# Kernel tuning notes

Hardware: AMD Instinct MI355X
Metric: run time of the kernel (lower is better)

Reference implementation:

```python
import jax, jax.numpy as jnp
import numpy as np

N = 100000
E = 300000
IN_C = 256
HID = 256   # 2 * out_channels
OUT_C = 128


def setup_inputs() -> dict:
    key = jax.random.key(0)
    k1, k2, k3, k4, k5 = jax.random.split(key, 5)
    x = jax.random.normal(k1, (N, IN_C), dtype=jnp.float32)
    edge_index = jax.random.randint(k2, (2, E), 0, N, dtype=jnp.int64)
    # Glorot-style init scale for GEMM weights
    W1 = jax.random.normal(k3, (IN_C, HID), dtype=jnp.float32) * (1.0 / np.sqrt(IN_C))
    b1 = jnp.zeros((HID,), dtype=jnp.float32)
    W2 = jax.random.normal(k4, (HID, OUT_C), dtype=jnp.float32) * (1.0 / np.sqrt(HID))
    b2 = jnp.zeros((OUT_C,), dtype=jnp.float32)
    return {"x": x, "edge_index": edge_index, "W1": W1, "b1": b1, "W2": W2, "b2": b2}


def _gcn_conv(x, W, b, src, dst, norm, n_nodes):
    # x: [N, Fin] -> transform then gather-scale-scatter aggregate
    h = x @ W                                   # [N, Fout]
    msgs = h[src] * norm[:, None]               # [E+N, Fout] (includes self-loops)
    out = jax.ops.segment_sum(msgs, dst, num_segments=n_nodes)
    return out + b


def _gcn_norm(edge_index, n_nodes):
    # add self-loops, compute symmetric deg^-1/2 normalization (PyG GCNConv default)
    loops = jnp.arange(n_nodes, dtype=edge_index.dtype)
    src = jnp.concatenate([edge_index[0], loops])
    dst = jnp.concatenate([edge_index[1], loops])
    deg = jax.ops.segment_sum(jnp.ones_like(dst, dtype=jnp.float32), dst, num_segments=n_nodes)
    dinv = jnp.where(deg > 0, jax.lax.rsqrt(deg), 0.0)
    norm = dinv[src] * dinv[dst]                # [E+N]
    return src, dst, norm


def reference(x, edge_index, W1, b1, W2, b2):
    n_nodes = x.shape[0]
    src, dst, norm = _gcn_norm(edge_index, n_nodes)
    h = _gcn_conv(x, W1, b1, src, dst, norm, n_nodes)
    h = jax.nn.relu(h)
    # dropout is identity in eval mode (reference baseline runs deterministic eval)
    return _gcn_conv(h, W2, b2, src, dst, norm, n_nodes)
```

## Files before the change

### kernel.cpp

```cpp
#include <hip/hip_runtime.h>
#include <stdint.h>

#define IN_C  256
#define HID   256
#define OUT_C 128
#define SCAN_BS 1024

typedef __bf16 bf16x8 __attribute__((ext_vector_type(8)));
typedef float  f32x4  __attribute__((ext_vector_type(4)));
typedef unsigned short u16x8 __attribute__((ext_vector_type(8)));
typedef unsigned short u16x4 __attribute__((ext_vector_type(4)));
typedef unsigned short u16x2 __attribute__((ext_vector_type(2)));
typedef unsigned int u32;

static __device__ __forceinline__ unsigned short f2b(float f) {
    union { float f; uint32_t u; } v; v.f = f;
    uint32_t r = v.u + 0x7fffu + ((v.u >> 16) & 1u);
    return (unsigned short)(r >> 16);
}
static __device__ __forceinline__ float b2f(unsigned short b) {
    union { uint32_t u; float f; } v; v.u = ((uint32_t)b) << 16;
    return v.f;
}
static __device__ __forceinline__ u32 cvtpk(float lo, float hi) {
    u32 r;
    asm("v_cvt_pk_bf16_f32 %0, %1, %2" : "=v"(r) : "v"(lo), "v"(hi));
    return r;
}

typedef __attribute__((address_space(1))) const u32 gas_u32;
typedef __attribute__((address_space(3))) u32 las_u32;
static __device__ __forceinline__ void gld16(const void* g, void* l) {
    __builtin_amdgcn_global_load_lds((gas_u32*)g, (las_u32*)l, 16, 0, 0);
}

__global__ void k_init(const float* __restrict__ W1, const float* __restrict__ W2,
                       unsigned short* __restrict__ W1T, unsigned short* __restrict__ W2T,
                       int* __restrict__ cnt, int n) {
    int i = blockIdx.x * blockDim.x + threadIdx.x;
    if (i < 65536) W1T[i] = f2b(W1[(i & 255) * HID + (i >> 8)]);
    if (i < 32768) W2T[i] = f2b(W2[(i & 255) * OUT_C + (i >> 8)]);
    if (i < n) cnt[i] = 0;
}

__global__ void k_count(const int* __restrict__ dst, int* __restrict__ cnt, int e) {
    int i = blockIdx.x * blockDim.x + threadIdx.x;
    if (i < e) atomicAdd(&cnt[dst[i]], 1);
}

__global__ __launch_bounds__(SCAN_BS) void k_scan_block(
    const int* __restrict__ cnt, int* __restrict__ rs, int* __restrict__ bsum, int n) {
    __shared__ int s[SCAN_BS];
    const int tid = threadIdx.x;
    const int i = blockIdx.x * SCAN_BS + tid;
    int v = (i < n) ? cnt[i] + 1 : 0;
    s[tid] = v;
    __syncthreads();
    for (int off = 1; off < SCAN_BS; off <<= 1) {
        int t = (tid >= off) ? s[tid - off] : 0;
        __syncthreads();
        s[tid] += t;
        __syncthreads();
    }
    if (i < n) rs[i] = s[tid] - v;
    if (tid == SCAN_BS - 1) bsum[blockIdx.x] = s[tid];
}

__global__ void k_scan_sums(int* __restrict__ bsum, int nb) {
    __shared__ int s[128];
    const int tid = threadIdx.x;
    int v = (tid < nb) ? bsum[tid] : 0;
    s[tid] = v;
    __syncthreads();
    for (int off = 1; off < 128; off <<= 1) {
        int t = (tid >= off) ? s[tid - off] : 0;
        __syncthreads();
        s[tid] += t;
        __syncthreads();
    }
    if (tid < nb) bsum[tid] = s[tid] - v;
}

__global__ void k_scan_add(int* __restrict__ rs, int* __restrict__ cur,
                           const int* __restrict__ bsum, const int* __restrict__ cnt,
                           float* __restrict__ dinv, int2* __restrict__ csrw, int n) {
    int i = blockIdx.x * blockDim.x + threadIdx.x;
    if (i < n) {
        int v = rs[i] + bsum[i >> 10];
        rs[i] = v;
        cur[i] = v + 1;
        float dp1 = (float)(cnt[i] + 1);
        dinv[i] = rsqrtf(dp1);
        csrw[v] = make_int2(i, __float_as_int(1.0f / dp1));
    }
}

__global__ void k_fill(const int* __restrict__ src, const int* __restrict__ dst,
                       const float* __restrict__ dinv,
                       int* __restrict__ cur, int2* __restrict__ csrw, int e) {
    int i = blockIdx.x * blockDim.x + threadIdx.x;
    if (i < e) {
        int s = src[i], d = dst[i];
        int p = atomicAdd(&cur[d], 1);
        csrw[p] = make_int2(s, __float_as_int(dinv[s] * dinv[d]));
    }
}

__global__ __launch_bounds__(256) void k_gemm1(
    const float* __restrict__ x, const unsigned short* __restrict__ W1T,
    unsigned short* __restrict__ t1, int n) {
    __shared__ __align__(16) unsigned short As[128 * 64];
    __shared__ __align__(16) unsigned short Bs[128 * 64];
    const int tid  = threadIdx.x;
    const int bm = blockIdx.x >> 1, bn = blockIdx.x & 1;
    const int row0 = bm * 128, col0 = bn * 128;
    const int wid = tid >> 6, lane = tid & 63;
    const int wm = wid >> 1, wn = wid & 1;
    const int lrow = lane & 15, lgrp = lane >> 4;

    f32x4 acc[4][4];
    #pragma unroll
    for (int i = 0; i < 4; ++i)
        #pragma unroll
        for (int j = 0; j < 4; ++j)
            acc[i][j] = (f32x4){0.f, 0.f, 0.f, 0.f};

    for (int kt = 0; kt < 4; ++kt) {
        #pragma unroll
        for (int i = 0; i < 4; ++i) {
            int chunk = tid + 256 * i;
            int nn = chunk >> 3, c = chunk & 7;
            gld16(&W1T[(size_t)(col0 + nn) * 256 + kt * 64 + ((c ^ (nn & 7)) * 8)],
                  &Bs[chunk * 8]);
        }
        #pragma unroll
        for (int i = 0; i < 4; ++i) {
            int chunk = tid + 256 * i;
            int r = chunk >> 3, c = chunk & 7;
            int grow = row0 + r;
            union { u32 w[4]; u16x8 v; } pk;
            pk.w[0] = 0; pk.w[1] = 0; pk.w[2] = 0; pk.w[3] = 0;
            if (grow < n) {
                const float* sp = x + (size_t)grow * IN_C + kt * 64 + c * 8;
                f32x4 a = *(const f32x4*)sp;
                f32x4 b = *(const f32x4*)(sp + 4);
                pk.w[0] = cvtpk(a[0], a[1]); pk.w[1] = cvtpk(a[2], a[3]);
                pk.w[2] = cvtpk(b[0], b[1]); pk.w[3] = cvtpk(b[2], b[3]);
            }
            *(u16x8*)&As[r * 64 + ((c ^ (r & 7)) * 8)] = pk.v;
        }
        __syncthreads();
        #pragma unroll
        for (int kk = 0; kk < 2; ++kk) {
            const int cfrag = kk * 4 + lgrp;
            bf16x8 av[4], bv[4];
            #pragma unroll
            for (int mf = 0; mf < 4; ++mf) {
                int r = wm * 64 + mf * 16 + lrow;
                av[mf] = *(const bf16x8*)&As[r * 64 + ((cfrag ^ (r & 7)) * 8)];
            }
            #pragma unroll
            for (int nf = 0; nf < 4; ++nf) {
                int cc = wn * 64 + nf * 16 + lrow;
                bv[nf] = *(const bf16x8*)&Bs[cc * 64 + ((cfrag ^ (cc & 7)) * 8)];
            }
            #pragma unroll
            for (int mf = 0; mf < 4; ++mf)
                #pragma unroll
                for (int nf = 0; nf < 4; ++nf)
                    acc[mf][nf] = __builtin_amdgcn_mfma_f32_16x16x32_bf16(
                        av[mf], bv[nf], acc[mf][nf], 0, 0, 0);
        }
        __syncthreads();
    }
    #pragma unroll
    for (int mf = 0; mf < 4; ++mf)
        #pragma unroll
        for (int j = 0; j < 4; ++j) {
            int grow = row0 + wm * 64 + mf * 16 + lgrp * 4 + j;
            if (grow < n) {
                #pragma unroll
                for (int nf = 0; nf < 4; ++nf) {
                    int col = col0 + wn * 64 + nf * 16 + lrow;
                    t1[(size_t)grow * HID + col] = f2b(acc[mf][nf][j]);
                }
            }
        }
}

__global__ __launch_bounds__(256) void k_agg1(
    const unsigned short* __restrict__ t1, const int* __restrict__ rs,
    const int* __restrict__ cnt, const int2* __restrict__ csrw,
    const float* __restrict__ b1, unsigned short* __restrict__ out1, int n) {
    const int w = blockIdx.x * 4 + (threadIdx.x >> 6);
    const int n0 = w * 4;
    if (n0 >= n) return;
    const int lane = threadIdx.x & 63;
    const int ch = lane * 4;
    int beg[4], m[4];
    #pragma unroll
    for (int q = 0; q < 4; ++q) {
        int node = n0 + q;
        bool valid = node < n;
        beg[q] = valid ? rs[node] : 0;
        m[q]   = valid ? cnt[node] + 1 : 0;
    }
    float acc[4][4];
    #pragma unroll
    for (int q = 0; q < 4; ++q)
        #pragma unroll
        for (int k = 0; k < 4; ++k) acc[q][k] = 0.f;
    const int m01 = m[0] > m[1] ? m[0] : m[1];
    const int m23 = m[2] > m[3] ? m[2] : m[3];
    const int mmax = m01 > m23 ? m01 : m23;
    for (int j = 0; j < mmax; ++j) {
        #pragma unroll
        for (int q = 0; q < 4; ++q) {
            if (j < m[q]) {
                int2 p = csrw[beg[q] + j];
                float wq = __int_as_float(p.y);
                u16x4 u = *(const u16x4*)&t1[(size_t)p.x * HID + ch];
                acc[q][0] += b2f(u[0]) * wq; acc[q][1] += b2f(u[1]) * wq;
                acc[q][2] += b2f(u[2]) * wq; acc[q][3] += b2f(u[3]) * wq;
            }
        }
    }
    float4 bb = *(const float4*)(b1 + ch);
    #pragma unroll
    for (int q = 0; q < 4; ++q) {
        int node = n0 + q;
        if (node < n) {
            u16x4 o;
            o[0] = f2b(fmaxf(acc[q][0] + bb.x, 0.f));
            o[1] = f2b(fmaxf(acc[q][1] + bb.y, 0.f));
            o[2] = f2b(fmaxf(acc[q][2] + bb.z, 0.f));
            o[3] = f2b(fmaxf(acc[q][3] + bb.w, 0.f));
            *(u16x4*)&out1[(size_t)node * HID + ch] = o;
        }
    }
}

__global__ __launch_bounds__(256) void k_gemm2(
    const unsigned short* __restrict__ out1, const unsigned short* __restrict__ W2T,
    unsigned short* __restrict__ t2, int n) {
    __shared__ __align__(16) unsigned short As[128 * 64];
    __shared__ __align__(16) unsigned short Bs[128 * 64];
    const int tid  = threadIdx.x;
    const int row0 = blockIdx.x * 128;
    const int wid = tid >> 6, lane = tid & 63;
    const int wm = wid >> 1, wn = wid & 1;
    const int lrow = lane & 15, lgrp = lane >> 4;

    f32x4 acc[4][4];
    #pragma unroll
    for (int i = 0; i < 4; ++i)
        #pragma unroll
        for (int j = 0; j < 4; ++j)
            acc[i][j] = (f32x4){0.f, 0.f, 0.f, 0.f};

    for (int kt = 0; kt < 4; ++kt) {
        #pragma unroll
        for (int i = 0; i < 4; ++i) {
            int chunk = tid + 256 * i;
            int r = chunk >> 3, c = chunk & 7;
            int grow = row0 + r; if (grow > n - 1) grow = n - 1;
            gld16(&out1[(size_t)grow * HID + kt * 64 + ((c ^ (r & 7)) * 8)],
                  &As[chunk * 8]);
        }
        #pragma unroll
        for (int i = 0; i < 4; ++i) {
            int chunk = tid + 256 * i;
            int nn = chunk >> 3, c = chunk & 7;
            gld16(&W2T[(size_t)nn * 256 + kt * 64 + ((c ^ (nn & 7)) * 8)],
                  &Bs[chunk * 8]);
        }
        __syncthreads();
        #pragma unroll
        for (int kk = 0; kk < 2; ++kk) {
            const int cfrag = kk * 4 + lgrp;
            bf16x8 av[4], bv[4];
            #pragma unroll
            for (int mf = 0; mf < 4; ++mf) {
                int r = wm * 64 + mf * 16 + lrow;
                av[mf] = *(const bf16x8*)&As[r * 64 + ((cfrag ^ (r & 7)) * 8)];
            }
            #pragma unroll
            for (int nf = 0; nf < 4; ++nf) {
                int cc = wn * 64 + nf * 16 + lrow;
                bv[nf] = *(const bf16x8*)&Bs[cc * 64 + ((cfrag ^ (cc & 7)) * 8)];
            }
            #pragma unroll
            for (int mf = 0; mf < 4; ++mf)
                #pragma unroll
                for (int nf = 0; nf < 4; ++nf)
                    acc[mf][nf] = __builtin_amdgcn_mfma_f32_16x16x32_bf16(
                        av[mf], bv[nf], acc[mf][nf], 0, 0, 0);
        }
        __syncthreads();
    }
    #pragma unroll
    for (int mf = 0; mf < 4; ++mf)
        #pragma unroll
        for (int j = 0; j < 4; ++j) {
            int grow = row0 + wm * 64 + mf * 16 + lgrp * 4 + j;
            if (grow < n) {
                #pragma unroll
                for (int nf = 0; nf < 4; ++nf) {
                    int col = wn * 64 + nf * 16 + lrow;
                    t2[(size_t)grow * OUT_C + col] = f2b(acc[mf][nf][j]);
                }
            }
        }
}

__global__ __launch_bounds__(256) void k_agg2(
    const unsigned short* __restrict__ t2, const int* __restrict__ rs,
    const int* __restrict__ cnt, const int2* __restrict__ csrw,
    const float* __restrict__ b2, float* __restrict__ out, int n) {
    const int w = blockIdx.x * 4 + (threadIdx.x >> 6);
    const int n0 = w * 4;
    if (n0 >= n) return;
    const int lane = threadIdx.x & 63;
    const int ch = lane * 2;
    int beg[4], m[4];
    #pragma unroll
    for (int q = 0; q < 4; ++q) {
        int node = n0 + q;
        bool valid = node < n;
        beg[q] = valid ? rs[node] : 0;
        m[q]   = valid ? cnt[node] + 1 : 0;
    }
    float acc[4][2];
    #pragma unroll
    for (int q = 0; q < 4; ++q) { acc[q][0] = 0.f; acc[q][1] = 0.f; }
    const int m01 = m[0] > m[1] ? m[0] : m[1];
    const int m23 = m[2] > m[3] ? m[2] : m[3];
    const int mmax = m01 > m23 ? m01 : m23;
    for (int j = 0; j < mmax; ++j) {
        #pragma unroll
        for (int q = 0; q < 4; ++q) {
            if (j < m[q]) {
                int2 p = csrw[beg[q] + j];
                float wq = __int_as_float(p.y);
                u16x2 u = *(const u16x2*)&t2[(size_t)p.x * OUT_C + ch];
                acc[q][0] += b2f(u[0]) * wq; acc[q][1] += b2f(u[1]) * wq;
            }
        }
    }
    float2 bb = *(const float2*)(b2 + ch);
    #pragma unroll
    for (int q = 0; q < 4; ++q) {
        int node = n0 + q;
        if (node < n)
            *(float2*)&out[(size_t)node * OUT_C + ch] =
                make_float2(acc[q][0] + bb.x, acc[q][1] + bb.y);
    }
}

extern "C" void kernel_launch(void* const* d_in, const int* in_sizes, int n_in,
                              void* d_out, int out_size, void* d_ws, size_t ws_size,
                              hipStream_t stream) {
    const float* x  = (const float*)d_in[0];
    const int*   ei = (const int*)d_in[1];
    const float* W1 = (const float*)d_in[2];
    const float* b1 = (const float*)d_in[3];
    const float* W2 = (const float*)d_in[4];
    const float* b2 = (const float*)d_in[5];
    float* out = (float*)d_out;

    const int n = in_sizes[0] / IN_C;
    const int e = in_sizes[1] / 2;
    const int* src = ei;
    const int* dst = ei + e;

    int*   cnt  = (int*)d_ws;
    int*   rs   = cnt + n;
    int*   cur  = rs + n;
    int*   bsum = cur + n;
    float* dinv = (float*)(bsum + 128);
    int2*  csrw = (int2*)(dinv + n);
    unsigned short* W1T = (unsigned short*)(csrw + (size_t)e + n);
    unsigned short* W2T = W1T + 65536;
    unsigned short* t1  = W2T + 32768;
    unsigned short* out1 = t1 + (size_t)n * HID;
    unsigned short* t2  = t1;

    const int nb = (n + SCAN_BS - 1) / SCAN_BS;

    k_init<<<(n + 255) / 256, 256, 0, stream>>>(W1, W2, W1T, W2T, cnt, n);
    k_count<<<(e + 255) / 256, 256, 0, stream>>>(dst, cnt, e);
    k_scan_block<<<nb, SCAN_BS, 0, stream>>>(cnt, rs, bsum, n);
    k_scan_sums<<<1, 128, 0, stream>>>(bsum, nb);
    k_scan_add<<<(n + 255) / 256, 256, 0, stream>>>(rs, cur, bsum, cnt, dinv, csrw, n);
    k_fill<<<(e + 255) / 256, 256, 0, stream>>>(src, dst, dinv, cur, csrw, e);

    const int mb = (n + 127) / 128;
    k_gemm1<<<mb * 2, 256, 0, stream>>>(x, W1T, t1, n);
    const int aggblk = (n + 15) / 16;
    k_agg1<<<aggblk, 256, 0, stream>>>(t1, rs, cnt, csrw, b1, out1, n);
    k_gemm2<<<mb, 256, 0, stream>>>(out1, W2T, t2, n);
    k_agg2<<<aggblk, 256, 0, stream>>>(t2, rs, cnt, csrw, b2, out, n);
}
```

Before: 218.1 us.

## Restructure GEMM1 into full-width 512-thread tiles with double-buffered LDS prefetch

GEMM1 now has each block compute all 256 output columns for 128 rows with 8 waves, so x is read once instead of twice (the old grid split N in two). The K loop uses 32-wide steps with double-buffered LDS, prefetching the next W1 tile via global_load_lds and the next x slice into registers while MFMAs run on the current buffer. W1 is pre-packed in a k-chunked layout that matches the LDS layout, and the XOR swizzle is replaced by a column-chunk-major layout. Out-of-range rows are clamped instead of zero-filled. The trade-offs are more LDS per block, more sync points and possible bank conflicts in the new layout.

```diff
diff --git a/kernel.cpp b/kernel.cpp
--- a/kernel.cpp
+++ b/kernel.cpp
@@ -35,10 +35,15 @@
 }
 
 __global__ void k_init(const float* __restrict__ W1, const float* __restrict__ W2,
-                       unsigned short* __restrict__ W1T, unsigned short* __restrict__ W2T,
+                       unsigned short* __restrict__ W1G, unsigned short* __restrict__ W2T,
                        int* __restrict__ cnt, int n) {
     int i = blockIdx.x * blockDim.x + threadIdx.x;
-    if (i < 65536) W1T[i] = f2b(W1[(i & 255) * HID + (i >> 8)]);
+    if (i < 65536) {
+        int gi = i >> 3, j = i & 7;
+        int kt = gi >> 10, c = (gi >> 8) & 3, nn = gi & 255;
+        int k = kt * 32 + c * 8 + j;
+        W1G[i] = f2b(W1[(size_t)k * HID + nn]);
+    }
     if (i < 32768) W2T[i] = f2b(W2[(i & 255) * OUT_C + (i >> 8)]);
     if (i < n) cnt[i] = 0;
 }
@@ -106,17 +111,20 @@
     }
 }
 
-__global__ __launch_bounds__(256) void k_gemm1(
-    const float* __restrict__ x, const unsigned short* __restrict__ W1T,
+__global__ __launch_bounds__(512) void k_gemm1(
+    const float* __restrict__ x, const unsigned short* __restrict__ W1G,
     unsigned short* __restrict__ t1, int n) {
-    __shared__ __align__(16) unsigned short As[128 * 64];
-    __shared__ __align__(16) unsigned short Bs[128 * 64];
+    __shared__ __align__(16) unsigned short As[2][4096];
+    __shared__ __align__(16) unsigned short Bs[2][8192];
     const int tid  = threadIdx.x;
-    const int bm = blockIdx.x >> 1, bn = blockIdx.x & 1;
-    const int row0 = bm * 128, col0 = bn * 128;
+    const int row0 = blockIdx.x * 128;
     const int wid = tid >> 6, lane = tid & 63;
-    const int wm = wid >> 1, wn = wid & 1;
+    const int wm = wid >> 2, wn = wid & 3;
     const int lrow = lane & 15, lgrp = lane >> 4;
+
+    const int ar = tid & 127, ac = tid >> 7;
+    int arow = row0 + ar; if (arow > n - 1) arow = n - 1;
+    const float* aptr = x + (size_t)arow * IN_C + ac * 8;
 
     f32x4 acc[4][4];
     #pragma unroll
@@ -125,54 +133,63 @@
         for (int j = 0; j < 4; ++j)
             acc[i][j] = (f32x4){0.f, 0.f, 0.f, 0.f};
 
-    for (int kt = 0; kt < 4; ++kt) {
-        #pragma unroll
-        for (int i = 0; i < 4; ++i) {
-            int chunk = tid + 256 * i;
-            int nn = chunk >> 3, c = chunk & 7;
-            gld16(&W1T[(size_t)(col0 + nn) * 256 + kt * 64 + ((c ^ (nn & 7)) * 8)],
-                  &Bs[chunk * 8]);
-        }
-        #pragma unroll
-        for (int i = 0; i < 4; ++i) {
-            int chunk = tid + 256 * i;
-            int r = chunk >> 3, c = chunk & 7;
-            int grow = row0 + r;
+    {
+        #pragma unroll
+        for (int i = 0; i < 2; ++i) {
+            int chunk = tid + 512 * i;
+            gld16(&W1G[(size_t)chunk * 8], &Bs[0][chunk * 8]);
+        }
+        f32x4 a = *(const f32x4*)aptr;
+        f32x4 b = *(const f32x4*)(aptr + 4);
+        union { u32 w[4]; u16x8 v; } pk;
+        pk.w[0] = cvtpk(a[0], a[1]); pk.w[1] = cvtpk(a[2], a[3]);
+        pk.w[2] = cvtpk(b[0], b[1]); pk.w[3] = cvtpk(b[2], b[3]);
+        *(u16x8*)&As[0][ac * 1024 + ar * 8] = pk.v;
+    }
+    __syncthreads();
+
+    int cur = 0;
+    for (int kt = 0; kt < 8; ++kt) {
+        const int nxt = cur ^ 1;
+        f32x4 pa, pb;
+        const bool more = (kt < 7);
+        if (more) {
+            #pragma unroll
+            for (int i = 0; i < 2; ++i) {
+                int chunk = tid + 512 * i;
+                gld16(&W1G[(size_t)(kt + 1) * 8192 + chunk * 8], &Bs[nxt][chunk * 8]);
+            }
+            const float* ap = aptr + (kt + 1) * 32;
+            pa = *(const f32x4*)ap;
+            pb = *(const f32x4*)(ap + 4);
+        }
+        bf16x8 av[4], bv[4];
+        #pragma unroll
+        for (int mf = 0; mf < 4; ++mf) {
+            int r = wm * 64 + mf * 16 + lrow;
+            av[mf] = *(const bf16x8*)&As[cur][lgrp * 1024 + r * 8];
+        }
+        #pragma unroll
+        for (int nf = 0; nf < 4; ++nf) {
+            int cc = wn * 64 + nf * 16 + lrow;
+            bv[nf] = *(const bf16x8*)&Bs[cur][lgrp * 2048 + cc * 8];
+        }
+        #pragma unroll
+        for (int mf = 0; mf < 4; ++mf)
+            #pragma unroll
+            for (int nf = 0; nf < 4; ++nf)
+                acc[mf][nf] = __builtin_amdgcn_mfma_f32_16x16x32_bf16(
+                    av[mf], bv[nf], acc[mf][nf], 0, 0, 0);
+        if (more) {
             union { u32 w[4]; u16x8 v; } pk;
-            pk.w[0] = 0; pk.w[1] = 0; pk.w[2] = 0; pk.w[3] = 0;
-            if (grow < n) {
-                const float* sp = x + (size_t)grow * IN_C + kt * 64 + c * 8;
-                f32x4 a = *(const f32x4*)sp;
-                f32x4 b = *(const f32x4*)(sp + 4);
-                pk.w[0] = cvtpk(a[0], a[1]); pk.w[1] = cvtpk(a[2], a[3]);
-                pk.w[2] = cvtpk(b[0], b[1]); pk.w[3] = cvtpk(b[2], b[3]);
-            }
-            *(u16x8*)&As[r * 64 + ((c ^ (r & 7)) * 8)] = pk.v;
-        }
-        __syncthreads();
-        #pragma unroll
-        for (int kk = 0; kk < 2; ++kk) {
-            const int cfrag = kk * 4 + lgrp;
-            bf16x8 av[4], bv[4];
-            #pragma unroll
-            for (int mf = 0; mf < 4; ++mf) {
-                int r = wm * 64 + mf * 16 + lrow;
-                av[mf] = *(const bf16x8*)&As[r * 64 + ((cfrag ^ (r & 7)) * 8)];
-            }
-            #pragma unroll
-            for (int nf = 0; nf < 4; ++nf) {
-                int cc = wn * 64 + nf * 16 + lrow;
-                bv[nf] = *(const bf16x8*)&Bs[cc * 64 + ((cfrag ^ (cc & 7)) * 8)];
-            }
-            #pragma unroll
-            for (int mf = 0; mf < 4; ++mf)
-                #pragma unroll
-                for (int nf = 0; nf < 4; ++nf)
-                    acc[mf][nf] = __builtin_amdgcn_mfma_f32_16x16x32_bf16(
-                        av[mf], bv[nf], acc[mf][nf], 0, 0, 0);
-        }
-        __syncthreads();
-    }
+            pk.w[0] = cvtpk(pa[0], pa[1]); pk.w[1] = cvtpk(pa[2], pa[3]);
+            pk.w[2] = cvtpk(pb[0], pb[1]); pk.w[3] = cvtpk(pb[2], pb[3]);
+            *(u16x8*)&As[nxt][ac * 1024 + ar * 8] = pk.v;
+        }
+        __syncthreads();
+        cur = nxt;
+    }
+
     #pragma unroll
     for (int mf = 0; mf < 4; ++mf)
         #pragma unroll
@@ -181,7 +198,7 @@
             if (grow < n) {
                 #pragma unroll
                 for (int nf = 0; nf < 4; ++nf) {
-                    int col = col0 + wn * 64 + nf * 16 + lrow;
+                    int col = wn * 64 + nf * 16 + lrow;
                     t1[(size_t)grow * HID + col] = f2b(acc[mf][nf][j]);
                 }
             }
@@ -379,15 +396,15 @@
     int*   bsum = cur + n;
     float* dinv = (float*)(bsum + 128);
     int2*  csrw = (int2*)(dinv + n);
-    unsigned short* W1T = (unsigned short*)(csrw + (size_t)e + n);
-    unsigned short* W2T = W1T + 65536;
+    unsigned short* W1G = (unsigned short*)(csrw + (size_t)e + n);
+    unsigned short* W2T = W1G + 65536;
     unsigned short* t1  = W2T + 32768;
     unsigned short* out1 = t1 + (size_t)n * HID;
     unsigned short* t2  = t1;
 
     const int nb = (n + SCAN_BS - 1) / SCAN_BS;
 
-    k_init<<<(n + 255) / 256, 256, 0, stream>>>(W1, W2, W1T, W2T, cnt, n);
+    k_init<<<(n + 255) / 256, 256, 0, stream>>>(W1, W2, W1G, W2T, cnt, n);
     k_count<<<(e + 255) / 256, 256, 0, stream>>>(dst, cnt, e);
     k_scan_block<<<nb, SCAN_BS, 0, stream>>>(cnt, rs, bsum, n);
     k_scan_sums<<<1, 128, 0, stream>>>(bsum, nb);
@@ -395,7 +412,7 @@
     k_fill<<<(e + 255) / 256, 256, 0, stream>>>(src, dst, dinv, cur, csrw, e);
 
     const int mb = (n + 127) / 128;
-    k_gemm1<<<mb * 2, 256, 0, stream>>>(x, W1T, t1, n);
+    k_gemm1<<<mb, 512, 0, stream>>>(x, W1G, t1, n);
     const int aggblk = (n + 15) / 16;
     k_agg1<<<aggblk, 256, 0, stream>>>(t1, rs, cnt, csrw, b1, out1, n);
     k_gemm2<<<mb, 256, 0, stream>>>(out1, W2T, t2, n);
```

Measured after the change: 209.4 us. 4.0% less time.
